# Optimization experiments

Hardware: AMD Instinct MI355X
Metric: run time of the kernel (lower is better)

The kernel has to match this reference:

```python
import jax, jax.numpy as jnp
import numpy as np

D = 768
H = 12
MLP = 3072
EPS = 1e-5


def _layernorm(x, g, b):
    mu = jnp.mean(x, axis=-1, keepdims=True)
    var = jnp.var(x, axis=-1, keepdims=True)
    return (x - mu) * jax.lax.rsqrt(var + EPS) * g + b


def setup_inputs() -> dict:
    key = jax.random.key(0)
    ks = jax.random.split(key, 16)
    s = 0.02
    inp = {
        "x": jax.random.normal(ks[0], (8, 1024, D), dtype=jnp.float32),
        "ln1_g": jnp.ones((D,), jnp.float32),
        "ln1_b": jnp.zeros((D,), jnp.float32),
        "Wq": jax.random.normal(ks[1], (D, D), jnp.float32) * s,
        "bq": jnp.zeros((D,), jnp.float32),
        "Wk": jax.random.normal(ks[2], (D, D), jnp.float32) * s,
        "bk": jnp.zeros((D,), jnp.float32),
        "Wv": jax.random.normal(ks[3], (D, D), jnp.float32) * s,
        "bv": jnp.zeros((D,), jnp.float32),
        "Wo": jax.random.normal(ks[4], (D, D), jnp.float32) * s,
        "bo": jnp.zeros((D,), jnp.float32),
        "ln2_g": jnp.ones((D,), jnp.float32),
        "ln2_b": jnp.zeros((D,), jnp.float32),
        "W1": jax.random.normal(ks[5], (D, MLP), jnp.float32) * s,
        "b1": jnp.zeros((MLP,), jnp.float32),
        "W2": jax.random.normal(ks[6], (MLP, D), jnp.float32) * s,
        "b2": jnp.zeros((D,), jnp.float32),
    }
    return inp


def reference(x, ln1_g, ln1_b, Wq, bq, Wk, bk, Wv, bv, Wo, bo, ln2_g, ln2_b, W1, b1, W2, b2):
    b, n, d = x.shape
    dh = d // H
    scale = 1.0 / jnp.sqrt(jnp.float32(d))  # NOTE: sqrt(input_dim), per source

    h = _layernorm(x, ln1_g, ln1_b)
    q = (h @ Wq + bq).reshape(b, n, H, dh).transpose(0, 2, 1, 3)  # bhnf
    k = (h @ Wk + bk).reshape(b, n, H, dh).transpose(0, 2, 1, 3)
    v = (h @ Wv + bv).reshape(b, n, H, dh).transpose(0, 2, 1, 3)

    score = jax.nn.softmax(jnp.einsum('bhif,bhjf->bhij', q, k) * scale, axis=-1)
    attn = jnp.einsum('bhij,bhjf->bihf', score, v).reshape(b, n, d)
    out = attn @ Wo + bo + x  # residual (dropout p=0)

    h2 = _layernorm(out, ln2_g, ln2_b)
    mlp = jax.nn.gelu(jax.nn.gelu(h2 @ W1 + b1, approximate=False) @ W2 + b2, approximate=False)
    return mlp + out
```

## Files before the change

### kernel.cpp

```cpp
#include <hip/hip_runtime.h>
#include <hip/hip_bf16.h>
#include <math.h>

typedef __bf16 bf16x8 __attribute__((ext_vector_type(8)));
typedef float f32x4 __attribute__((ext_vector_type(4)));

#define DD 768
#define HH 12
#define MLPD 3072
#define QSCALE 0.036084391824351615f

__device__ __forceinline__ float gelu_fast(float x) {
    float y = 1.5957691216057308f * x + 0.07135481283154893f * x * x * x;
    return x * __builtin_amdgcn_rcpf(1.0f + __expf(-y));
}

__device__ __forceinline__ void gload16(const void* g, void* l) {
    __builtin_amdgcn_global_load_lds(
        (const __attribute__((address_space(1))) unsigned int*)g,
        (__attribute__((address_space(3))) unsigned int*)l, 16, 0, 0);
}

__global__ __launch_bounds__(256) void wtrans_all(
    const float* __restrict__ Wq, const float* __restrict__ Wk,
    const float* __restrict__ Wv, const float* __restrict__ Wo,
    const float* __restrict__ W1, const float* __restrict__ W2,
    __bf16* __restrict__ wqkv, __bf16* __restrict__ wo,
    __bf16* __restrict__ w1, __bf16* __restrict__ w2) {
    __shared__ float tile[64][65];
    int b = blockIdx.x;
    const float* W; __bf16* Wt; int K, N, tk, tn;
    if (b < 432) {
        int wsel = b / 144, r = b - wsel * 144;
        W = wsel == 0 ? Wq : (wsel == 1 ? Wk : Wv);
        Wt = wqkv + (size_t)wsel * 768 * 768;
        K = 768; N = 768; tk = r % 12; tn = r / 12;
    } else if (b < 576) {
        int r = b - 432; W = Wo; Wt = wo; K = 768; N = 768; tk = r % 12; tn = r / 12;
    } else if (b < 1152) {
        int r = b - 576; W = W1; Wt = w1; K = 768; N = 3072; tk = r % 12; tn = r / 12;
    } else {
        int r = b - 1152; W = W2; Wt = w2; K = 3072; N = 768; tk = r % 48; tn = r / 48;
    }
    int k0 = tk * 64, n0 = tn * 64;
    int t = threadIdx.x;
    int tr = t >> 6, tc = t & 63;
#pragma unroll
    for (int i = 0; i < 16; ++i) {
        int row = i * 4 + tr;
        tile[row][tc] = W[(size_t)(k0 + row) * N + n0 + tc];
    }
    __syncthreads();
#pragma unroll
    for (int i = 0; i < 16; ++i) {
        int row = i * 4 + tr;
        Wt[(size_t)(n0 + row) * K + k0 + tc] = (__bf16)tile[tc][row];
    }
}

__global__ __launch_bounds__(64) void ln_kernel(const float* __restrict__ X,
                                                const float* __restrict__ g,
                                                const float* __restrict__ b,
                                                __bf16* __restrict__ O) {
    int row = blockIdx.x;
    int lane = threadIdx.x;
    const float* xr = X + (size_t)row * DD;
    float4 v[3];
    float s = 0.f, ss = 0.f;
#pragma unroll
    for (int i = 0; i < 3; ++i) {
        v[i] = *reinterpret_cast<const float4*>(&xr[(i * 64 + lane) * 4]);
        s += v[i].x + v[i].y + v[i].z + v[i].w;
        ss += v[i].x * v[i].x + v[i].y * v[i].y + v[i].z * v[i].z + v[i].w * v[i].w;
    }
#pragma unroll
    for (int m = 1; m < 64; m <<= 1) {
        s += __shfl_xor(s, m);
        ss += __shfl_xor(ss, m);
    }
    float mu = s * (1.0f / DD);
    float rstd = rsqrtf(ss * (1.0f / DD) - mu * mu + 1e-5f);
#pragma unroll
    for (int i = 0; i < 3; ++i) {
        int c = (i * 64 + lane) * 4;
        float4 gv = *reinterpret_cast<const float4*>(&g[c]);
        float4 bv = *reinterpret_cast<const float4*>(&b[c]);
        union { __bf16 h[4]; uint2 u; } o;
        o.h[0] = (__bf16)((v[i].x - mu) * rstd * gv.x + bv.x);
        o.h[1] = (__bf16)((v[i].y - mu) * rstd * gv.y + bv.y);
        o.h[2] = (__bf16)((v[i].z - mu) * rstd * gv.z + bv.z);
        o.h[3] = (__bf16)((v[i].w - mu) * rstd * gv.w + bv.w);
        *reinterpret_cast<uint2*>(&O[(size_t)row * DD + c]) = o.u;
    }
}

template <int EPI>
__global__ __launch_bounds__(512, 2) void gemm8(
    const __bf16* __restrict__ A, const __bf16* __restrict__ Bt,
    const float* __restrict__ b0, const float* __restrict__ b1, const float* __restrict__ b2,
    void* __restrict__ o0, void* __restrict__ o1, void* __restrict__ o2,
    int M, int N, int K) {
    extern __shared__ __bf16 lds[];
    __bf16* As = lds;
    __bf16* Bs = lds + 49152;
    const int t = threadIdx.x;
    const int w = t >> 6, lane = t & 63;
    const int wm = w >> 1, wn = w & 1;
    const int lr = lane & 15, lg = lane >> 4;
    const int m0 = blockIdx.x * 256, n0 = blockIdx.y * 128;
    const int lrow8 = lane >> 3;
    const int cSwz = ((lane & 7) ^ lrow8) * 8;

    const __bf16* aSrc = A + (size_t)(m0 + w * 32 + lrow8) * K + cSwz;
    const __bf16* bSrc = Bt + (size_t)(n0 + w * 16 + lrow8) * K + cSwz;
    const int ldsA = w * 32 * 64;
    const int ldsB = w * 16 * 64;

    const int nt = K >> 6;
    f32x4 acc[4][4] = {};

    auto stageA = [&](int T, int c) {
        gload16(aSrc + (size_t)(c * 8) * K + T * 64,
                &As[(T % 3) * 16384 + ldsA + c * 8 * 64]);
    };
    auto stageB = [&](int T, int c) {
        gload16(bSrc + (size_t)(c * 8) * K + T * 64,
                &Bs[(T % 3) * 8192 + ldsB + c * 8 * 64]);
    };

    for (int T = 0; T < 2; ++T) {
        stageA(T, 0); stageA(T, 1); stageA(T, 2); stageA(T, 3);
        stageB(T, 0); stageB(T, 1);
    }
    asm volatile("s_waitcnt vmcnt(6)" ::: "memory");
    __builtin_amdgcn_s_barrier();

    for (int T = 0; T < nt; ++T) {
        const int bufA = (T % 3) * 16384, bufB = (T % 3) * 8192;
#pragma unroll
        for (int kg = 0; kg < 2; ++kg) {
            bf16x8 af[4], bfr[4];
#pragma unroll
            for (int i = 0; i < 4; ++i)
                af[i] = *reinterpret_cast<const bf16x8*>(
                    &As[bufA + (wm * 64 + i * 16 + lr) * 64 + (((kg << 2) | lg) ^ (lr & 7)) * 8]);
#pragma unroll
            for (int j = 0; j < 4; ++j)
                bfr[j] = *reinterpret_cast<const bf16x8*>(
                    &Bs[bufB + (wn * 64 + j * 16 + lr) * 64 + (((kg << 2) | lg) ^ (lr & 7)) * 8]);
            if (T + 2 < nt) {
                stageA(T + 2, kg * 2); stageA(T + 2, kg * 2 + 1); stageB(T + 2, kg);
            }
            __builtin_amdgcn_s_barrier();
            asm volatile("s_waitcnt lgkmcnt(0)" ::: "memory");
            __builtin_amdgcn_sched_barrier(0);
            __builtin_amdgcn_s_setprio(1);
#pragma unroll
            for (int i = 0; i < 4; ++i)
#pragma unroll
                for (int j = 0; j < 4; ++j)
                    acc[i][j] = __builtin_amdgcn_mfma_f32_16x16x32_bf16(bfr[j], af[i], acc[i][j], 0, 0, 0);
            __builtin_amdgcn_s_setprio(0);
            if (kg == 1) {
                if (T < nt - 2) { asm volatile("s_waitcnt vmcnt(6)" ::: "memory"); }
                else            { asm volatile("s_waitcnt vmcnt(0)" ::: "memory"); }
            }
            __builtin_amdgcn_s_barrier();
        }
    }

#pragma unroll
    for (int i = 0; i < 4; ++i) {
        const int m = m0 + wm * 64 + i * 16 + lr;
        const int bI = m >> 10, ntok = m & 1023;
#pragma unroll
        for (int j = 0; j < 4; ++j) {
            const int n = n0 + wn * 64 + j * 16 + lg * 4;
            if (EPI == 0) {
                const int wid = n / 768;
                const int cc0 = n - wid * 768;
                const int hh = cc0 >> 6, f0 = cc0 & 63;
                const float* bsel = (wid == 0 ? b0 : (wid == 1 ? b1 : b2));
                const float4 bv = *reinterpret_cast<const float4*>(&bsel[cc0]);
                const float v0 = acc[i][j][0] + bv.x, v1 = acc[i][j][1] + bv.y;
                const float v2 = acc[i][j][2] + bv.z, v3 = acc[i][j][3] + bv.w;
                if (wid == 0) {
                    union { __bf16 h[4]; uint2 u; } pk;
                    pk.h[0] = (__bf16)(v0 * QSCALE); pk.h[1] = (__bf16)(v1 * QSCALE);
                    pk.h[2] = (__bf16)(v2 * QSCALE); pk.h[3] = (__bf16)(v3 * QSCALE);
                    *reinterpret_cast<uint2*>(
                        &((__bf16*)o0)[((((size_t)(bI * HH + hh) << 10) + ntok) << 6) + f0]) = pk.u;
                } else if (wid == 1) {
                    union { __bf16 h[4]; uint2 u; } pk;
                    pk.h[0] = (__bf16)v0; pk.h[1] = (__bf16)v1;
                    pk.h[2] = (__bf16)v2; pk.h[3] = (__bf16)v3;
                    *reinterpret_cast<uint2*>(
                        &((__bf16*)o1)[((((size_t)(bI * HH + hh) << 10) + ntok) << 6) + f0]) = pk.u;
                } else {
                    __bf16* vb = (__bf16*)o2;
                    size_t base = ((size_t)(bI * HH + hh) * 64 + f0) << 10;
                    vb[base + ntok] = (__bf16)v0;
                    vb[base + (1 << 10) + ntok] = (__bf16)v1;
                    vb[base + (2 << 10) + ntok] = (__bf16)v2;
                    vb[base + (3 << 10) + ntok] = (__bf16)v3;
                }
            } else {
                const float4 bv = *reinterpret_cast<const float4*>(&b0[n]);
                union { __bf16 h[4]; uint2 u; } pk;
                pk.h[0] = (__bf16)gelu_fast(acc[i][j][0] + bv.x);
                pk.h[1] = (__bf16)gelu_fast(acc[i][j][1] + bv.y);
                pk.h[2] = (__bf16)gelu_fast(acc[i][j][2] + bv.z);
                pk.h[3] = (__bf16)gelu_fast(acc[i][j][3] + bv.w);
                *reinterpret_cast<uint2*>(&((__bf16*)o0)[(size_t)m * MLPD + n]) = pk.u;
            }
        }
    }
}

template <int EPI>
__global__ __launch_bounds__(256, 2) void gemm_p3(
    const __bf16* __restrict__ A, const __bf16* __restrict__ Bt,
    const float* __restrict__ b0, void* __restrict__ o0,
    const float* __restrict__ resid, int M, int N, int K) {
    extern __shared__ __bf16 lds[];
    __bf16* As = lds;
    __bf16* Bs = lds + 16384;
    const int t = threadIdx.x;
    const int w = t >> 6, lane = t & 63;
    const int wm = w >> 1, wn = w & 1;
    const int lr = lane & 15, lg = lane >> 4;
    const int m0 = blockIdx.x * 128, n0 = blockIdx.y * 128;
    const int lrow8 = lane >> 3;
    const int cSwz = ((lane & 7) ^ lrow8) * 8;

    const __bf16* aSrc = A + (size_t)(m0 + w * 32 + lrow8) * K + cSwz;
    const __bf16* bSrc = Bt + (size_t)(n0 + w * 32 + lrow8) * K + cSwz;
    const int ldsW = w * 32 * 64;

    const int nt = K >> 6;
    f32x4 acc[4][4] = {};

    auto stage = [&](int T) {
        const int buf = (T & 1) * 8192;
#pragma unroll
        for (int c = 0; c < 4; ++c)
            gload16(aSrc + (size_t)(c * 8) * K + T * 64, &As[buf + ldsW + c * 8 * 64]);
#pragma unroll
        for (int c = 0; c < 4; ++c)
            gload16(bSrc + (size_t)(c * 8) * K + T * 64, &Bs[buf + ldsW + c * 8 * 64]);
    };

    stage(0);
    for (int T = 0; T < nt; ++T) {
        if (T + 1 < nt) {
            stage(T + 1);
            asm volatile("s_waitcnt vmcnt(8)" ::: "memory");
        } else {
            asm volatile("s_waitcnt vmcnt(0)" ::: "memory");
        }
        __builtin_amdgcn_s_barrier();
        const int buf = (T & 1) * 8192;
#pragma unroll
        for (int kg = 0; kg < 2; ++kg) {
            bf16x8 af[4], bfr[4];
#pragma unroll
            for (int i = 0; i < 4; ++i)
                af[i] = *reinterpret_cast<const bf16x8*>(
                    &As[buf + (wm * 64 + i * 16 + lr) * 64 + (((kg << 2) | lg) ^ (lr & 7)) * 8]);
#pragma unroll
            for (int j = 0; j < 4; ++j)
                bfr[j] = *reinterpret_cast<const bf16x8*>(
                    &Bs[buf + (wn * 64 + j * 16 + lr) * 64 + (((kg << 2) | lg) ^ (lr & 7)) * 8]);
            asm volatile("s_waitcnt lgkmcnt(0)" ::: "memory");
            __builtin_amdgcn_sched_barrier(0);
            __builtin_amdgcn_s_setprio(1);
#pragma unroll
            for (int i = 0; i < 4; ++i)
#pragma unroll
                for (int j = 0; j < 4; ++j)
                    acc[i][j] = __builtin_amdgcn_mfma_f32_16x16x32_bf16(bfr[j], af[i], acc[i][j], 0, 0, 0);
            __builtin_amdgcn_s_setprio(0);
        }
        __builtin_amdgcn_s_barrier();
    }

#pragma unroll
    for (int i = 0; i < 4; ++i) {
        const int m = m0 + wm * 64 + i * 16 + lr;
#pragma unroll
        for (int j = 0; j < 4; ++j) {
            const int n = n0 + wn * 64 + j * 16 + lg * 4;
            const float4 bv = *reinterpret_cast<const float4*>(&b0[n]);
            const float v0 = acc[i][j][0] + bv.x, v1 = acc[i][j][1] + bv.y;
            const float v2 = acc[i][j][2] + bv.z, v3 = acc[i][j][3] + bv.w;
            const float4 rv = *reinterpret_cast<const float4*>(&resid[(size_t)m * DD + n]);
            if (EPI == 2) {
                float4 ov = {v0 + rv.x, v1 + rv.y, v2 + rv.z, v3 + rv.w};
                *reinterpret_cast<float4*>(&((float*)o0)[(size_t)m * DD + n]) = ov;
            } else {
                float4 ov = {gelu_fast(v0) + rv.x, gelu_fast(v1) + rv.y,
                             gelu_fast(v2) + rv.z, gelu_fast(v3) + rv.w};
                *reinterpret_cast<float4*>(&((float*)o0)[(size_t)m * DD + n]) = ov;
            }
        }
    }
}

__global__ __launch_bounds__(512, 6) void attn_kernel(
    const __bf16* __restrict__ Q, const __bf16* __restrict__ Kg,
    const __bf16* __restrict__ Vt, __bf16* __restrict__ Aout) {
    __shared__ char KsB[2][64 * 128];
    __shared__ char VsB[2][64 * 128];
    __shared__ char PsB[8][16 * 128];
    const int id = blockIdx.x;
    const int swz = (id & 7) * 96 + (id >> 3);
    const int bh = swz >> 3, qt = swz & 7;
    const int t = threadIdx.x, w = t >> 6, lane = t & 63;
    const int lr = lane & 15, lg = lane >> 4;
    const size_t bhN = (size_t)bh << 10;
    const int q0 = qt * 128;

    bf16x8 qf[2];
#pragma unroll
    for (int kg = 0; kg < 2; ++kg)
        qf[kg] = *reinterpret_cast<const bf16x8*>(&Q[(bhN + q0 + w * 16 + lr) * 64 + kg * 32 + lg * 8]);

    const int srow = t >> 3;
    const int sc = ((t & 7) ^ (srow & 7)) * 16;
    const char* kbase = (const char*)Kg + bhN * 128;
    const char* vbase = (const char*)Vt + ((size_t)bh << 17);
    const int wlds = w * 1024;

    f32x4 oacc[4] = {};
    float lsum[4] = {0.f, 0.f, 0.f, 0.f};

    gload16(kbase + (size_t)srow * 128 + sc, KsB[0] + wlds);
    gload16(vbase + (size_t)srow * 2048 + sc, VsB[0] + wlds);

    for (int kt = 0; kt < 16; ++kt) {
        const int buf = kt & 1;
        if (kt < 15) {
            gload16(kbase + (size_t)((kt + 1) * 64 + srow) * 128 + sc, KsB[buf ^ 1] + wlds);
            gload16(vbase + (size_t)srow * 2048 + (kt + 1) * 128 + sc, VsB[buf ^ 1] + wlds);
            asm volatile("s_waitcnt vmcnt(2)" ::: "memory");
        } else {
            asm volatile("s_waitcnt vmcnt(0)" ::: "memory");
        }
        __builtin_amdgcn_s_barrier();

        f32x4 s[4] = {};
        __builtin_amdgcn_s_setprio(1);
#pragma unroll
        for (int kg = 0; kg < 2; ++kg) {
#pragma unroll
            for (int j = 0; j < 4; ++j) {
                int row = j * 16 + lr;
                bf16x8 kf = *reinterpret_cast<const bf16x8*>(
                    KsB[buf] + ((row * 128 + kg * 64 + lg * 16) ^ ((row & 7) << 4)));
                s[j] = __builtin_amdgcn_mfma_f32_16x16x32_bf16(qf[kg], kf, s[j], 0, 0, 0);
            }
        }
        __builtin_amdgcn_s_setprio(0);
#pragma unroll
        for (int r = 0; r < 4; ++r) {
            int prow = lg * 4 + r;
#pragma unroll
            for (int j = 0; j < 4; ++j) {
                float pv = __expf(s[j][r]);
                lsum[r] += pv;
                *reinterpret_cast<__bf16*>(
                    PsB[w] + ((prow * 128 + (j * 16 + lr) * 2) ^ ((prow & 7) << 4))) = (__bf16)pv;
            }
        }
        __builtin_amdgcn_s_setprio(1);
#pragma unroll
        for (int kg = 0; kg < 2; ++kg) {
            bf16x8 pf = *reinterpret_cast<const bf16x8*>(
                PsB[w] + ((lr * 128 + kg * 64 + lg * 16) ^ ((lr & 7) << 4)));
#pragma unroll
            for (int j = 0; j < 4; ++j) {
                int row = j * 16 + lr;
                bf16x8 vf = *reinterpret_cast<const bf16x8*>(
                    VsB[buf] + ((row * 128 + kg * 64 + lg * 16) ^ ((row & 7) << 4)));
                oacc[j] = __builtin_amdgcn_mfma_f32_16x16x32_bf16(pf, vf, oacc[j], 0, 0, 0);
            }
        }
        __builtin_amdgcn_s_setprio(0);
        __builtin_amdgcn_s_barrier();
    }

#pragma unroll
    for (int r = 0; r < 4; ++r)
#pragma unroll
        for (int m = 1; m < 16; m <<= 1) lsum[r] += __shfl_xor(lsum[r], m);

    const int bI = bh / HH, hh = bh % HH;
#pragma unroll
    for (int r = 0; r < 4; ++r) {
        float inv = 1.0f / lsum[r];
        int qrow = q0 + w * 16 + lg * 4 + r;
        size_t base = ((size_t)(bI << 10) + qrow) * DD + hh * 64;
#pragma unroll
        for (int j = 0; j < 4; ++j)
            Aout[base + j * 16 + lr] = (__bf16)(oacc[j][r] * inv);
    }
}

extern "C" void kernel_launch(void* const* d_in, const int* in_sizes, int n_in,
                              void* d_out, int out_size, void* d_ws, size_t ws_size,
                              hipStream_t stream) {
    const float* x     = (const float*)d_in[0];
    const float* ln1_g = (const float*)d_in[1];
    const float* ln1_b = (const float*)d_in[2];
    const float* Wq    = (const float*)d_in[3];
    const float* bq    = (const float*)d_in[4];
    const float* Wk    = (const float*)d_in[5];
    const float* bk    = (const float*)d_in[6];
    const float* Wv    = (const float*)d_in[7];
    const float* bv    = (const float*)d_in[8];
    const float* Wo    = (const float*)d_in[9];
    const float* bo    = (const float*)d_in[10];
    const float* ln2_g = (const float*)d_in[11];
    const float* ln2_b = (const float*)d_in[12];
    const float* W1    = (const float*)d_in[13];
    const float* b1    = (const float*)d_in[14];
    const float* W2    = (const float*)d_in[15];
    const float* b2    = (const float*)d_in[16];

    char* p = (char*)d_ws;
    auto alloc = [&](size_t bytes) { char* r = p; p += bytes; return r; };
    __bf16* wqkv_t = (__bf16*)alloc((size_t)2304 * 768 * 2);
    __bf16* wo_t   = (__bf16*)alloc((size_t)768 * 768 * 2);
    __bf16* w1_t   = (__bf16*)alloc((size_t)3072 * 768 * 2);
    __bf16* w2_t   = (__bf16*)alloc((size_t)768 * 3072 * 2);
    __bf16* h      = (__bf16*)alloc((size_t)8192 * 768 * 2);
    float*  outb   = (float*) alloc((size_t)8192 * 768 * 4);
    __bf16* q      = (__bf16*)alloc((size_t)8192 * 768 * 2);
    __bf16* kb     = (__bf16*)alloc((size_t)8192 * 768 * 2);
    __bf16* vt     = (__bf16*)alloc((size_t)8192 * 768 * 2);
    __bf16* attn   = (__bf16*)alloc((size_t)8192 * 768 * 2);
    __bf16* mid    = q;

    const int LDS8 = 147456;
    const int LDSP = 65536;
    hipFuncSetAttribute(reinterpret_cast<const void*>(gemm8<0>),
                        hipFuncAttributeMaxDynamicSharedMemorySize, LDS8);
    hipFuncSetAttribute(reinterpret_cast<const void*>(gemm8<3>),
                        hipFuncAttributeMaxDynamicSharedMemorySize, LDS8);
    hipFuncSetAttribute(reinterpret_cast<const void*>(gemm_p3<2>),
                        hipFuncAttributeMaxDynamicSharedMemorySize, LDSP);
    hipFuncSetAttribute(reinterpret_cast<const void*>(gemm_p3<4>),
                        hipFuncAttributeMaxDynamicSharedMemorySize, LDSP);

    wtrans_all<<<1728, 256, 0, stream>>>(Wq, Wk, Wv, Wo, W1, W2, wqkv_t, wo_t, w1_t, w2_t);

    ln_kernel<<<8192, 64, 0, stream>>>(x, ln1_g, ln1_b, h);
    gemm8<0><<<dim3(32, 18), 512, LDS8, stream>>>(h, wqkv_t, bq, bk, bv, q, kb, vt,
                                                  8192, 2304, 768);
    attn_kernel<<<768, 512, 0, stream>>>(q, kb, vt, attn);
    gemm_p3<2><<<dim3(64, 6), 256, LDSP, stream>>>(attn, wo_t, bo, outb, x, 8192, 768, 768);
    ln_kernel<<<8192, 64, 0, stream>>>(outb, ln2_g, ln2_b, h);
    gemm8<3><<<dim3(32, 24), 512, LDS8, stream>>>(h, w1_t, b1, nullptr, nullptr, mid,
                                                  nullptr, nullptr, 8192, 3072, 768);
    gemm_p3<4><<<dim3(64, 6), 256, LDSP, stream>>>(mid, w2_t, b2, (float*)d_out, outb,
                                                   8192, 768, 3072);
}
```

Baseline: 247.2 us.

## Unify all GEMMs on 128x128 double-buffered 256-thread kernel

Replaces the 256x128-tile, 512-thread, triple-buffered GEMM used for the QKV and first MLP projections with the 128x128, 256-thread, double-buffered kernel already used for the output and second MLP projections. All four epilogues now live in one template. Smaller tiles and less LDS give more blocks and better occupancy. The cost is lower data reuse per block and a shallower prefetch pipeline, which can expose memory latency.

After: 239.6 us. -3.0%, faster.

```diff
diff --git a/kernel.cpp b/kernel.cpp
--- a/kernel.cpp
+++ b/kernel.cpp
@@ -95,63 +95,60 @@
 }
 
 template <int EPI>
-__global__ __launch_bounds__(512, 2) void gemm8(
+__global__ __launch_bounds__(256, 2) void gemm_pl(
     const __bf16* __restrict__ A, const __bf16* __restrict__ Bt,
     const float* __restrict__ b0, const float* __restrict__ b1, const float* __restrict__ b2,
     void* __restrict__ o0, void* __restrict__ o1, void* __restrict__ o2,
-    int M, int N, int K) {
+    const float* __restrict__ resid, int M, int N, int K) {
     extern __shared__ __bf16 lds[];
     __bf16* As = lds;
-    __bf16* Bs = lds + 49152;
+    __bf16* Bs = lds + 16384;
     const int t = threadIdx.x;
     const int w = t >> 6, lane = t & 63;
     const int wm = w >> 1, wn = w & 1;
     const int lr = lane & 15, lg = lane >> 4;
-    const int m0 = blockIdx.x * 256, n0 = blockIdx.y * 128;
+    const int m0 = blockIdx.x * 128, n0 = blockIdx.y * 128;
     const int lrow8 = lane >> 3;
     const int cSwz = ((lane & 7) ^ lrow8) * 8;
 
     const __bf16* aSrc = A + (size_t)(m0 + w * 32 + lrow8) * K + cSwz;
-    const __bf16* bSrc = Bt + (size_t)(n0 + w * 16 + lrow8) * K + cSwz;
-    const int ldsA = w * 32 * 64;
-    const int ldsB = w * 16 * 64;
+    const __bf16* bSrc = Bt + (size_t)(n0 + w * 32 + lrow8) * K + cSwz;
+    const int ldsW = w * 32 * 64;
 
     const int nt = K >> 6;
     f32x4 acc[4][4] = {};
 
-    auto stageA = [&](int T, int c) {
-        gload16(aSrc + (size_t)(c * 8) * K + T * 64,
-                &As[(T % 3) * 16384 + ldsA + c * 8 * 64]);
+    auto stage = [&](int T) {
+        const int buf = (T & 1) * 8192;
+#pragma unroll
+        for (int c = 0; c < 4; ++c)
+            gload16(aSrc + (size_t)(c * 8) * K + T * 64, &As[buf + ldsW + c * 8 * 64]);
+#pragma unroll
+        for (int c = 0; c < 4; ++c)
+            gload16(bSrc + (size_t)(c * 8) * K + T * 64, &Bs[buf + ldsW + c * 8 * 64]);
     };
-    auto stageB = [&](int T, int c) {
-        gload16(bSrc + (size_t)(c * 8) * K + T * 64,
-                &Bs[(T % 3) * 8192 + ldsB + c * 8 * 64]);
-    };
-
-    for (int T = 0; T < 2; ++T) {
-        stageA(T, 0); stageA(T, 1); stageA(T, 2); stageA(T, 3);
-        stageB(T, 0); stageB(T, 1);
-    }
-    asm volatile("s_waitcnt vmcnt(6)" ::: "memory");
-    __builtin_amdgcn_s_barrier();
-
+
+    stage(0);
     for (int T = 0; T < nt; ++T) {
-        const int bufA = (T % 3) * 16384, bufB = (T % 3) * 8192;
+        if (T + 1 < nt) {
+            stage(T + 1);
+            asm volatile("s_waitcnt vmcnt(8)" ::: "memory");
+        } else {
+            asm volatile("s_waitcnt vmcnt(0)" ::: "memory");
+        }
+        __builtin_amdgcn_s_barrier();
+        const int buf = (T & 1) * 8192;
 #pragma unroll
         for (int kg = 0; kg < 2; ++kg) {
             bf16x8 af[4], bfr[4];
 #pragma unroll
             for (int i = 0; i < 4; ++i)
                 af[i] = *reinterpret_cast<const bf16x8*>(
-                    &As[bufA + (wm * 64 + i * 16 + lr) * 64 + (((kg << 2) | lg) ^ (lr & 7)) * 8]);
+                    &As[buf + (wm * 64 + i * 16 + lr) * 64 + (((kg << 2) | lg) ^ (lr & 7)) * 8]);
 #pragma unroll
             for (int j = 0; j < 4; ++j)
                 bfr[j] = *reinterpret_cast<const bf16x8*>(
-                    &Bs[bufB + (wn * 64 + j * 16 + lr) * 64 + (((kg << 2) | lg) ^ (lr & 7)) * 8]);
-            if (T + 2 < nt) {
-                stageA(T + 2, kg * 2); stageA(T + 2, kg * 2 + 1); stageB(T + 2, kg);
-            }
-            __builtin_amdgcn_s_barrier();
+                    &Bs[buf + (wn * 64 + j * 16 + lr) * 64 + (((kg << 2) | lg) ^ (lr & 7)) * 8]);
             asm volatile("s_waitcnt lgkmcnt(0)" ::: "memory");
             __builtin_amdgcn_sched_barrier(0);
             __builtin_amdgcn_s_setprio(1);
@@ -161,12 +158,8 @@
                 for (int j = 0; j < 4; ++j)
                     acc[i][j] = __builtin_amdgcn_mfma_f32_16x16x32_bf16(bfr[j], af[i], acc[i][j], 0, 0, 0);
             __builtin_amdgcn_s_setprio(0);
-            if (kg == 1) {
-                if (T < nt - 2) { asm volatile("s_waitcnt vmcnt(6)" ::: "memory"); }
-                else            { asm volatile("s_waitcnt vmcnt(0)" ::: "memory"); }
-            }
-            __builtin_amdgcn_s_barrier();
-        }
+        }
+        __builtin_amdgcn_s_barrier();
     }
 
 #pragma unroll
@@ -204,7 +197,7 @@
                     vb[base + (2 << 10) + ntok] = (__bf16)v2;
                     vb[base + (3 << 10) + ntok] = (__bf16)v3;
                 }
-            } else {
+            } else if (EPI == 3) {
                 const float4 bv = *reinterpret_cast<const float4*>(&b0[n]);
                 union { __bf16 h[4]; uint2 u; } pk;
                 pk.h[0] = (__bf16)gelu_fast(acc[i][j][0] + bv.x);
@@ -212,95 +205,19 @@
                 pk.h[2] = (__bf16)gelu_fast(acc[i][j][2] + bv.z);
                 pk.h[3] = (__bf16)gelu_fast(acc[i][j][3] + bv.w);
                 *reinterpret_cast<uint2*>(&((__bf16*)o0)[(size_t)m * MLPD + n]) = pk.u;
-            }
-        }
-    }
-}
-
-template <int EPI>
-__global__ __launch_bounds__(256, 2) void gemm_p3(
-    const __bf16* __restrict__ A, const __bf16* __restrict__ Bt,
-    const float* __restrict__ b0, void* __restrict__ o0,
-    const float* __restrict__ resid, int M, int N, int K) {
-    extern __shared__ __bf16 lds[];
-    __bf16* As = lds;
-    __bf16* Bs = lds + 16384;
-    const int t = threadIdx.x;
-    const int w = t >> 6, lane = t & 63;
-    const int wm = w >> 1, wn = w & 1;
-    const int lr = lane & 15, lg = lane >> 4;
-    const int m0 = blockIdx.x * 128, n0 = blockIdx.y * 128;
-    const int lrow8 = lane >> 3;
-    const int cSwz = ((lane & 7) ^ lrow8) * 8;
-
-    const __bf16* aSrc = A + (size_t)(m0 + w * 32 + lrow8) * K + cSwz;
-    const __bf16* bSrc = Bt + (size_t)(n0 + w * 32 + lrow8) * K + cSwz;
-    const int ldsW = w * 32 * 64;
-
-    const int nt = K >> 6;
-    f32x4 acc[4][4] = {};
-
-    auto stage = [&](int T) {
-        const int buf = (T & 1) * 8192;
-#pragma unroll
-        for (int c = 0; c < 4; ++c)
-            gload16(aSrc + (size_t)(c * 8) * K + T * 64, &As[buf + ldsW + c * 8 * 64]);
-#pragma unroll
-        for (int c = 0; c < 4; ++c)
-            gload16(bSrc + (size_t)(c * 8) * K + T * 64, &Bs[buf + ldsW + c * 8 * 64]);
-    };
-
-    stage(0);
-    for (int T = 0; T < nt; ++T) {
-        if (T + 1 < nt) {
-            stage(T + 1);
-            asm volatile("s_waitcnt vmcnt(8)" ::: "memory");
-        } else {
-            asm volatile("s_waitcnt vmcnt(0)" ::: "memory");
-        }
-        __builtin_amdgcn_s_barrier();
-        const int buf = (T & 1) * 8192;
-#pragma unroll
-        for (int kg = 0; kg < 2; ++kg) {
-            bf16x8 af[4], bfr[4];
-#pragma unroll
-            for (int i = 0; i < 4; ++i)
-                af[i] = *reinterpret_cast<const bf16x8*>(
-                    &As[buf + (wm * 64 + i * 16 + lr) * 64 + (((kg << 2) | lg) ^ (lr & 7)) * 8]);
-#pragma unroll
-            for (int j = 0; j < 4; ++j)
-                bfr[j] = *reinterpret_cast<const bf16x8*>(
-                    &Bs[buf + (wn * 64 + j * 16 + lr) * 64 + (((kg << 2) | lg) ^ (lr & 7)) * 8]);
-            asm volatile("s_waitcnt lgkmcnt(0)" ::: "memory");
-            __builtin_amdgcn_sched_barrier(0);
-            __builtin_amdgcn_s_setprio(1);
-#pragma unroll
-            for (int i = 0; i < 4; ++i)
-#pragma unroll
-                for (int j = 0; j < 4; ++j)
-                    acc[i][j] = __builtin_amdgcn_mfma_f32_16x16x32_bf16(bfr[j], af[i], acc[i][j], 0, 0, 0);
-            __builtin_amdgcn_s_setprio(0);
-        }
-        __builtin_amdgcn_s_barrier();
-    }
-
-#pragma unroll
-    for (int i = 0; i < 4; ++i) {
-        const int m = m0 + wm * 64 + i * 16 + lr;
-#pragma unroll
-        for (int j = 0; j < 4; ++j) {
-            const int n = n0 + wn * 64 + j * 16 + lg * 4;
-            const float4 bv = *reinterpret_cast<const float4*>(&b0[n]);
-            const float v0 = acc[i][j][0] + bv.x, v1 = acc[i][j][1] + bv.y;
-            const float v2 = acc[i][j][2] + bv.z, v3 = acc[i][j][3] + bv.w;
-            const float4 rv = *reinterpret_cast<const float4*>(&resid[(size_t)m * DD + n]);
-            if (EPI == 2) {
-                float4 ov = {v0 + rv.x, v1 + rv.y, v2 + rv.z, v3 + rv.w};
-                *reinterpret_cast<float4*>(&((float*)o0)[(size_t)m * DD + n]) = ov;
             } else {
-                float4 ov = {gelu_fast(v0) + rv.x, gelu_fast(v1) + rv.y,
-                             gelu_fast(v2) + rv.z, gelu_fast(v3) + rv.w};
-                *reinterpret_cast<float4*>(&((float*)o0)[(size_t)m * DD + n]) = ov;
+                const float4 bv = *reinterpret_cast<const float4*>(&b0[n]);
+                const float v0 = acc[i][j][0] + bv.x, v1 = acc[i][j][1] + bv.y;
+                const float v2 = acc[i][j][2] + bv.z, v3 = acc[i][j][3] + bv.w;
+                const float4 rv = *reinterpret_cast<const float4*>(&resid[(size_t)m * DD + n]);
+                if (EPI == 2) {
+                    float4 ov = {v0 + rv.x, v1 + rv.y, v2 + rv.z, v3 + rv.w};
+                    *reinterpret_cast<float4*>(&((float*)o0)[(size_t)m * DD + n]) = ov;
+                } else {
+                    float4 ov = {gelu_fast(v0) + rv.x, gelu_fast(v1) + rv.y,
+                                 gelu_fast(v2) + rv.z, gelu_fast(v3) + rv.w};
+                    *reinterpret_cast<float4*>(&((float*)o0)[(size_t)m * DD + n]) = ov;
+                }
             }
         }
     }
@@ -441,27 +358,27 @@
     __bf16* attn   = (__bf16*)alloc((size_t)8192 * 768 * 2);
     __bf16* mid    = q;
 
-    const int LDS8 = 147456;
     const int LDSP = 65536;
-    hipFuncSetAttribute(reinterpret_cast<const void*>(gemm8<0>),
-                        hipFuncAttributeMaxDynamicSharedMemorySize, LDS8);
-    hipFuncSetAttribute(reinterpret_cast<const void*>(gemm8<3>),
-                        hipFuncAttributeMaxDynamicSharedMemorySize, LDS8);
-    hipFuncSetAttribute(reinterpret_cast<const void*>(gemm_p3<2>),
+    hipFuncSetAttribute(reinterpret_cast<const void*>(gemm_pl<0>),
                         hipFuncAttributeMaxDynamicSharedMemorySize, LDSP);
-    hipFuncSetAttribute(reinterpret_cast<const void*>(gemm_p3<4>),
+    hipFuncSetAttribute(reinterpret_cast<const void*>(gemm_pl<2>),
                         hipFuncAttributeMaxDynamicSharedMemorySize, LDSP);
+    hipFuncSetAttribute(reinterpret_cast<const void*>(gemm_pl<3>),
+                        hipFuncAttributeMaxDynamicSharedMemorySize, LDSP);
+    hipFuncSetAttribute(reinterpret_cast<const void*>(gemm_pl<4>),
+                        hipFuncAttributeMaxDynamicSharedMemorySize, LDSP);
 
     wtrans_all<<<1728, 256, 0, stream>>>(Wq, Wk, Wv, Wo, W1, W2, wqkv_t, wo_t, w1_t, w2_t);
 
     ln_kernel<<<8192, 64, 0, stream>>>(x, ln1_g, ln1_b, h);
-    gemm8<0><<<dim3(32, 18), 512, LDS8, stream>>>(h, wqkv_t, bq, bk, bv, q, kb, vt,
-                                                  8192, 2304, 768);
+    gemm_pl<0><<<dim3(64, 18), 256, LDSP, stream>>>(h, wqkv_t, bq, bk, bv, q, kb, vt,
+                                                    nullptr, 8192, 2304, 768);
     attn_kernel<<<768, 512, 0, stream>>>(q, kb, vt, attn);
-    gemm_p3<2><<<dim3(64, 6), 256, LDSP, stream>>>(attn, wo_t, bo, outb, x, 8192, 768, 768);
+    gemm_pl<2><<<dim3(64, 6), 256, LDSP, stream>>>(attn, wo_t, bo, nullptr, nullptr, outb,
+                                                   nullptr, nullptr, x, 8192, 768, 768);
     ln_kernel<<<8192, 64, 0, stream>>>(outb, ln2_g, ln2_b, h);
-    gemm8<3><<<dim3(32, 24), 512, LDS8, stream>>>(h, w1_t, b1, nullptr, nullptr, mid,
-                                                  nullptr, nullptr, 8192, 3072, 768);
-    gemm_p3<4><<<dim3(64, 6), 256, LDSP, stream>>>(mid, w2_t, b2, (float*)d_out, outb,
-                                                   8192, 768, 3072);
-}
+    gemm_pl<3><<<dim3(64, 24), 256, LDSP, stream>>>(h, w1_t, b1, nullptr, nullptr, mid,
+                                                    nullptr, nullptr, nullptr, 8192, 3072, 768);
+    gemm_pl<4><<<dim3(64, 6), 256, LDSP, stream>>>(mid, w2_t, b2, nullptr, nullptr, (float*)d_out,
+                                                   nullptr, nullptr, outb, 8192, 768, 3072);
+}
```
